# Kernel tuning notes

Measured on AMD Instinct MI355X. Metric: run time of the kernel, lower is better.

The kernel has to match this reference:

```python
import jax, jax.numpy as jnp
import numpy as np

# ---- model constants (match init_kwargs) ----
B, N, T, L = 16384, 32, 300, 1
DIM = 2                      # len(state_index)
DT = 1.0 / (T * L)           # dt = 1/(T*l)
STEPS = T * L                # Euler integration steps (time_steps = STEPS+1)
A_X = 1.0                    # canonical DMP phase constant
TAU = 1.0
HID = 64
OUT = N * DIM + DIM          # fc2_mean output size


def setup_inputs() -> dict:
    key = jax.random.key(0)
    ks = jax.random.split(key, 8)
    s = lambda i, shape, scale: jax.random.normal(ks[i], shape, jnp.float32) * scale
    inp = {
        "state": jax.random.normal(ks[0], (B, 3), jnp.float32),
        "fc1_w": s(1, (HID, 3), 0.3),
        "fc1_b": jnp.full((HID,), 0.1, jnp.float32),
        "fc2m_w": s(2, (OUT, HID), 0.1),
        "fc2m_b": jnp.full((OUT,), 0.1, jnp.float32),
        "sig_w": s(3, (DIM, HID), 0.1),
        "sig_b": jnp.zeros((DIM,), jnp.float32),
        "val_w": s(4, (DIM, HID), 0.1),
        "val_b": jnp.zeros((DIM,), jnp.float32),
    }
    # DMPParameters: gaussian RBF centers on exp-decayed phase, canonical widths
    c = jnp.exp(-A_X * jnp.linspace(0.0, 1.0, N))
    inp["dmp_c"] = c.astype(jnp.float32)
    inp["dmp_sigma2"] = (N ** 1.5 / c / A_X).astype(jnp.float32)
    return inp


def dmp_rollout(w, goal, y0, dy0, a_z, c, sigma2):
    """Euler rollout of DMP transformation system.
    w: [M,N] basis weights, goal/y0/dy0/a_z: [M] per-channel scalars.
    Returns Y, dY, ddY each [M, STEPS+1]."""
    z0 = dy0 * TAU
    b_z = a_z / 4.0

    def step(carry, _):
        x, y, z = carry
        x = x + (-A_X * x) * TAU * DT                       # phase update
        psi = jnp.exp(-0.5 * (x - c) ** 2 / sigma2)          # [N] gaussian RBF
        fx = (w @ psi) * x * (goal - y0) / jnp.sum(psi)      # [M] forcing term
        dz = a_z * (b_z * (goal - y) - z) + fx
        dy = z
        y = y + TAU * dy * DT
        z = z + TAU * dz * DT
        return (x, y, z), (y, dy * TAU, dz * TAU)

    _, (Ys, dYs, ddYs) = jax.lax.scan(
        step, (jnp.float32(1.0), y0, z0), None, length=STEPS)
    Y = jnp.concatenate([y0[None], Ys], axis=0).T            # [M, STEPS+1]
    dY = jnp.concatenate([dy0[None], dYs], axis=0).T
    ddY = jnp.concatenate([z0[None], ddYs], axis=0).T
    return Y, dY, ddY


def reference(state, fc1_w, fc1_b, fc2m_w, fc2m_b, sig_w, sig_b,
              val_w, val_b, dmp_c, dmp_sigma2):
    x = jnp.tanh(state @ fc1_w.T + fc1_b) * 0.1              # [B,64]
    y0 = state[:, :DIM].reshape(-1)                           # [M=B*DIM]
    dy0 = jnp.zeros_like(y0) + 0.01

    # value = fc2_value(x).repeat(1,T).view(-1,T,2).transpose(1,2) == broadcast over T
    v = x @ val_w.T + val_b                                   # [B,2]
    value = jnp.broadcast_to(v[:, :, None], (B, DIM, T))

    sigma = (jax.nn.sigmoid(x @ sig_w.T + sig_b) * 1.0 + 0.001).reshape(-1, DIM, 1)

    ndp_wg = x @ fc2m_w.T + fc2m_b                            # [B, 2N+2]
    goal = ndp_wg[:, :DIM].reshape(-1)                        # [M]
    w = ndp_wg[:, DIM:DIM * (N + 1)].reshape(-1, N)           # [M,N]
    a_z = jnp.clip(ndp_wg[:, -1], 0.5, 30.0)                  # learned a_z (az=True)
    a_z = jnp.broadcast_to(a_z[:, None], (B, DIM)).reshape(-1)

    Y, _, _ = dmp_rollout(w, goal, y0, dy0, a_z, dmp_c, dmp_sigma2)
    y = Y.reshape(B, DIM, -1)[:, :, ::L]                      # [B,2,T+1]
    a = y[:, :, 1:] - y[:, :, :-1]                            # [B,2,T]
    return (a, sigma, value)
```

## Files before the change

### kernel.cpp

```cpp
#include <hip/hip_runtime.h>
#include <hip/hip_bf16.h>

#define NB 32
#define TS 300
#define NBATCH 16384
#define DTF (1.0f/300.0f)
#define A_ELEMS (NBATCH*2*TS)

typedef __attribute__((ext_vector_type(8))) short bf16x8;
typedef __attribute__((ext_vector_type(4))) float f32x4;

static __device__ __forceinline__ ushort f2bf(float f) {
    union { __hip_bfloat16 h; ushort u; } cv;
    cv.h = __float2bfloat16(f);
    return cv.u;
}


__global__ __launch_bounds__(256) void k_head(
    const float* __restrict__ state,
    const float* __restrict__ fc1_w, const float* __restrict__ fc1_b,
    const float* __restrict__ fc2m_w, const float* __restrict__ fc2m_b,
    const float* __restrict__ sig_w, const float* __restrict__ sig_b,
    const float* __restrict__ val_w, const float* __restrict__ val_b,
    const float* __restrict__ dmp_c, const float* __restrict__ dmp_s2,
    float* __restrict__ sig_out, float* __restrict__ pbuf,
    ushort* __restrict__ wbuf16, uint4* __restrict__ wsPhi)
{
    const int tid = threadIdx.x;
    if (blockIdx.x == 256) {
        const float l2 = log2f(1.0f - DTF);
        for (int t = tid; t < 304; t += 256) {
            ushort row[NB];
            if (t < TS) {
                const float x = exp2f((float)(t + 1) * l2);
                float ps[NB]; float s = 0.0f;
                #pragma unroll
                for (int n = 0; n < NB; ++n) {
                    float d = x - dmp_c[n];
                    float p = __expf(-0.5f * d * d / dmp_s2[n]);
                    ps[n] = p; s += p;
                }
                const float inv = x / s;
                #pragma unroll
                for (int n = 0; n < NB; ++n) row[n] = f2bf(ps[n] * inv);
            } else {
                #pragma unroll
                for (int n = 0; n < NB; ++n) row[n] = 0;
            }
            #pragma unroll
            for (int g0 = 0; g0 < 4; ++g0) {
                union { ushort us[8]; uint4 v; } pk;
                #pragma unroll
                for (int e = 0; e < 8; ++e) pk.us[e] = row[g0*8 + e];
                wsPhi[(t >> 4)*64 + g0*16 + (t & 15)] = pk.v;
            }
        }
        return;
    }

    __shared__ uint4 bfr[640];
    __shared__ float f1s[64*4];
    __shared__ float biasl[80];
    __shared__ float hlds[4*16*68];
    __shared__ float ct[4*16*84];
    __shared__ float scl[4][16][2];

    const int wv  = tid >> 6;
    const int l   = tid & 63;
    const int b16 = l & 15;
    const int g   = l >> 4;

    for (int e = tid; e < 640; e += 256) {
        const int T = e >> 7, kk = (e >> 6) & 1, lane = e & 63;
        const int r = T*16 + (lane & 15);
        const int k0 = kk*32 + (lane >> 4)*8;
        union { ushort us[8]; uint4 v; } pk;
        if (r < 70) {
            const float* src = (r < 66) ? (fc2m_w + r*64 + k0)
                             : (r < 68) ? (sig_w + (r-66)*64 + k0)
                             : (val_w + (r-68)*64 + k0);
            #pragma unroll
            for (int i = 0; i < 8; ++i) pk.us[i] = f2bf(src[i]);
        } else {
            #pragma unroll
            for (int i = 0; i < 8; ++i) pk.us[i] = 0;
        }
        bfr[e] = pk.v;
    }
    if (tid < 64) {
        f1s[tid*4+0] = fc1_w[tid*3+0];
        f1s[tid*4+1] = fc1_w[tid*3+1];
        f1s[tid*4+2] = fc1_w[tid*3+2];
        f1s[tid*4+3] = fc1_b[tid];
    }
    if (tid < 80) biasl[tid] = (tid < 66) ? fc2m_b[tid] : (tid < 68) ? sig_b[tid-66]
                             : (tid < 70) ? val_b[tid-68] : 0.0f;
    __syncthreads();

    const int bbase = blockIdx.x*64 + wv*16;
    const int bglob = bbase + b16;
    const float s0 = state[bglob*3+0], s1 = state[bglob*3+1], s2 = state[bglob*3+2];

    float* hrow = hlds + wv*1088 + b16*68;
    #pragma unroll
    for (int i = 0; i < 16; ++i) {
        const int hid = g + 4*i;
        const float4 fw = *(const float4*)(f1s + hid*4);
        const float pre = fmaf(fw.x, s0, fmaf(fw.y, s1, fmaf(fw.z, s2, fw.w)));
        const float e = __expf(2.0f * pre);
        hrow[hid] = (1.0f - 2.0f/(e + 1.0f)) * 0.1f;
    }

    bf16x8 A0, A1;
    {
        const float* hr = hlds + wv*1088 + b16*68 + g*8;
        const float4 h0 = *(const float4*)(hr),      h1 = *(const float4*)(hr + 4);
        const float4 h2 = *(const float4*)(hr + 32), h3 = *(const float4*)(hr + 36);
        union { bf16x8 v; ushort u[8]; } p0, p1;
        p0.u[0]=f2bf(h0.x); p0.u[1]=f2bf(h0.y); p0.u[2]=f2bf(h0.z); p0.u[3]=f2bf(h0.w);
        p0.u[4]=f2bf(h1.x); p0.u[5]=f2bf(h1.y); p0.u[6]=f2bf(h1.z); p0.u[7]=f2bf(h1.w);
        p1.u[0]=f2bf(h2.x); p1.u[1]=f2bf(h2.y); p1.u[2]=f2bf(h2.z); p1.u[3]=f2bf(h2.w);
        p1.u[4]=f2bf(h3.x); p1.u[5]=f2bf(h3.y); p1.u[6]=f2bf(h3.z); p1.u[7]=f2bf(h3.w);
        A0 = p0.v; A1 = p1.v;
    }

    float* ctw = ct + wv*1344;
    const f32x4 zacc = {0.0f, 0.0f, 0.0f, 0.0f};
    #pragma unroll
    for (int T = 0; T < 5; ++T) {
        union { uint4 q; bf16x8 v; } B0, B1;
        B0.q = bfr[(T*2+0)*64 + l];
        B1.q = bfr[(T*2+1)*64 + l];
        f32x4 acc = __builtin_amdgcn_mfma_f32_16x16x32_bf16(A0, B0.v, zacc, 0, 0, 0);
        acc = __builtin_amdgcn_mfma_f32_16x16x32_bf16(A1, B1.v, acc, 0, 0, 0);
        const int r = T*16 + b16;
        const float bs = biasl[r];
        #pragma unroll
        for (int reg = 0; reg < 4; ++reg)
            ctw[(g*4 + reg)*84 + r] = acc[reg] + bs;
    }

    if (l < 32) {
        const int b = l & 15, d = l >> 4;
        const float goal = ctw[b*84 + d];
        const float y0 = state[(bbase + b)*3 + d];
        scl[wv][b][d] = DTF * (goal - y0);
    }

    uint* wout = (uint*)wbuf16;
    #pragma unroll 1
    for (int b = 0; b < 16; ++b) {
        if (l < 32) {
            const float2 wp = *(const float2*)(ctw + b*84 + 2 + 2*l);
            const float sc = scl[wv][b][l >> 4];
            wout[(bbase + b)*32 + l] =
                (uint)f2bf(wp.x * sc) | ((uint)f2bf(wp.y * sc) << 16);
        }
    }
    if (l < 16) {
        const float* cb = ctw + l*84;
        const float az = fminf(fmaxf(cb[65], 0.5f), 30.0f);
        const float y0 = state[(bbase + l)*3 + 0];
        *(float4*)(pbuf + ((bbase + l)*2 + 0)*4) = make_float4(cb[0], az, y0, cb[68]);
    } else if (l < 32) {
        const int b = l - 16;
        const float* cb = ctw + b*84;
        const float az = fminf(fmaxf(cb[65], 0.5f), 30.0f);
        const float y0 = state[(bbase + b)*3 + 1];
        *(float4*)(pbuf + ((bbase + b)*2 + 1)*4) = make_float4(cb[1], az, y0, cb[69]);
    } else if (l < 48) {
        const int b = l - 32;
        const float* cb = ctw + b*84;
        const float sg0 = 1.0f / (1.0f + __expf(-cb[66])) + 0.001f;
        const float sg1 = 1.0f / (1.0f + __expf(-cb[67])) + 0.001f;
        *(float2*)(sig_out + (bbase + b)*2) = make_float2(sg0, sg1);
    }
}

__global__ __launch_bounds__(256) void k_roll(
    const uint4* __restrict__ wsPhi, const float* __restrict__ pbuf,
    const ushort* __restrict__ wbuf16, float* __restrict__ a_out,
    float* __restrict__ v_out)
{
    const int tid = threadIdx.x;
    const int wv = tid >> 6;
    const int j  = tid & 63;
    const int ch = j & 15;
    const int g  = j >> 4;
    const int m  = (blockIdx.x << 6) + (wv << 4) + ch;

    const float4 pp = *(const float4*)(pbuf + m*4);
    const float az = pp.y;
    const float Ac = (DTF * 0.25f) * az * az;
    const float OmB = fmaf(-DTF, az, 1.0f);
    const float c0 = Ac * pp.x;
    float y = pp.z;
    float z = 0.01f;
    const f32x4 cvec = {c0, c0, c0, c0};

    const bf16x8 wb = *(const bf16x8*)(wbuf16 + m*NB + g*8);
    const bf16x8* ap = (const bf16x8*)wsPhi;
    bf16x8 af = ap[j];

    float* aptr = a_out + m*TS + (g << 2);
    float* vptr = v_out + m*TS + (g << 2);
    const float4 vsp = make_float4(pp.w, pp.w, pp.w, pp.w);

    for (int c = 0; c < 19; ++c) {
        const bool st = (c < 18) | (g < 3);
        if (st) { *(float4*)vptr = vsp; }
        vptr += 16;

        f32x4 facc = __builtin_amdgcn_mfma_f32_16x16x32_bf16(af, wb, cvec, 0, 0, 0);
        if (c < 18) af = ap[(c + 1)*64 + j];

        float F[16];
        #pragma unroll
        for (int q = 0; q < 4; ++q) {
            float a = facc[q], b = facc[q];
            asm volatile("v_permlane16_swap_b32 %0, %1" : "+v"(a), "+v"(b));
            float a2 = a, b2 = b;
            asm volatile("v_permlane32_swap_b32 %0, %1" : "+v"(a), "+v"(a2));
            asm volatile("v_permlane32_swap_b32 %0, %1" : "+v"(b), "+v"(b2));
            F[0*4+q] = a; F[1*4+q] = b; F[2*4+q] = a2; F[3*4+q] = b2;
        }

        float avq[4];
        #pragma unroll
        for (int i = 0; i < 16; ++i) {
            const float t2 = fmaf(-Ac, y, F[i]);
            if (g == (i >> 2)) avq[i & 3] = z;
            y = fmaf(DTF, z, y);
            z = fmaf(OmB, z, t2);
        }

        if (st) {
            *(float4*)aptr = make_float4(avq[0]*DTF, avq[1]*DTF, avq[2]*DTF, avq[3]*DTF);
        }
        aptr += 16;
    }
}

extern "C" void kernel_launch(void* const* d_in, const int* in_sizes, int n_in,
                              void* d_out, int out_size, void* d_ws, size_t ws_size,
                              hipStream_t stream) {
    (void)in_sizes; (void)n_in; (void)out_size; (void)ws_size;
    const float* state  = (const float*)d_in[0];
    const float* fc1_w  = (const float*)d_in[1];
    const float* fc1_b  = (const float*)d_in[2];
    const float* fc2m_w = (const float*)d_in[3];
    const float* fc2m_b = (const float*)d_in[4];
    const float* sig_w  = (const float*)d_in[5];
    const float* sig_b  = (const float*)d_in[6];
    const float* val_w  = (const float*)d_in[7];
    const float* val_b  = (const float*)d_in[8];
    const float* dmp_c  = (const float*)d_in[9];
    const float* dmp_s2 = (const float*)d_in[10];

    float* out     = (float*)d_out;
    float* a_out   = out;
    float* sig_out = out + A_ELEMS;
    float* v_out   = out + A_ELEMS + NBATCH*2;

    char* ws = (char*)d_ws;
    uint4*  wsPhi  = (uint4*)ws;
    float*  pbuf   = (float*)(ws + 32768);
    ushort* wbuf16 = (ushort*)(ws + 557056);

    k_head<<<dim3(257), dim3(256), 0, stream>>>(state, fc1_w, fc1_b, fc2m_w, fc2m_b,
                                                sig_w, sig_b, val_w, val_b,
                                                dmp_c, dmp_s2,
                                                sig_out, pbuf, wbuf16, wsPhi);
    k_roll<<<dim3(512), dim3(256), 0, stream>>>(wsPhi, pbuf, wbuf16, a_out, v_out);
}
```

Before: 30.03 us.

## Fuse head and rollout kernels into one cooperative launch with grid sync

```diff
diff --git a/kernel.cpp b/kernel.cpp
--- a/kernel.cpp
+++ b/kernel.cpp
@@ -1,5 +1,8 @@
 #include <hip/hip_runtime.h>
 #include <hip/hip_bf16.h>
+#include <hip/hip_cooperative_groups.h>
+
+namespace cg = cooperative_groups;
 
 #define NB 32
 #define TS 300
@@ -17,7 +20,7 @@
 }
 
 
-__global__ __launch_bounds__(256) void k_head(
+__global__ __launch_bounds__(256) void k_all(
     const float* __restrict__ state,
     const float* __restrict__ fc1_w, const float* __restrict__ fc1_b,
     const float* __restrict__ fc2m_w, const float* __restrict__ fc2m_b,
@@ -25,10 +28,20 @@
     const float* __restrict__ val_w, const float* __restrict__ val_b,
     const float* __restrict__ dmp_c, const float* __restrict__ dmp_s2,
     float* __restrict__ sig_out, float* __restrict__ pbuf,
-    ushort* __restrict__ wbuf16, uint4* __restrict__ wsPhi)
+    ushort* __restrict__ wbuf16, uint4* __restrict__ wsPhi,
+    float* __restrict__ a_out, float* __restrict__ v_out)
 {
+    __shared__ uint4 bfr[640];
+    __shared__ float f1s[64*4];
+    __shared__ float biasl[80];
+    __shared__ float hlds[4*16*68];
+    __shared__ float ct[4*16*84];
+    __shared__ float scl[4][16][2];
+
     const int tid = threadIdx.x;
-    if (blockIdx.x == 256) {
+    const int bid = blockIdx.x;
+
+    if (bid == 256) {
         const float l2 = log2f(1.0f - DTF);
         for (int t = tid; t < 304; t += 256) {
             ushort row[NB];
@@ -56,189 +69,178 @@
                 wsPhi[(t >> 4)*64 + g0*16 + (t & 15)] = pk.v;
             }
         }
-        return;
-    }
-
-    __shared__ uint4 bfr[640];
-    __shared__ float f1s[64*4];
-    __shared__ float biasl[80];
-    __shared__ float hlds[4*16*68];
-    __shared__ float ct[4*16*84];
-    __shared__ float scl[4][16][2];
-
-    const int wv  = tid >> 6;
-    const int l   = tid & 63;
-    const int b16 = l & 15;
-    const int g   = l >> 4;
-
-    for (int e = tid; e < 640; e += 256) {
-        const int T = e >> 7, kk = (e >> 6) & 1, lane = e & 63;
-        const int r = T*16 + (lane & 15);
-        const int k0 = kk*32 + (lane >> 4)*8;
-        union { ushort us[8]; uint4 v; } pk;
-        if (r < 70) {
-            const float* src = (r < 66) ? (fc2m_w + r*64 + k0)
-                             : (r < 68) ? (sig_w + (r-66)*64 + k0)
-                             : (val_w + (r-68)*64 + k0);
-            #pragma unroll
-            for (int i = 0; i < 8; ++i) pk.us[i] = f2bf(src[i]);
-        } else {
-            #pragma unroll
-            for (int i = 0; i < 8; ++i) pk.us[i] = 0;
-        }
-        bfr[e] = pk.v;
-    }
-    if (tid < 64) {
-        f1s[tid*4+0] = fc1_w[tid*3+0];
-        f1s[tid*4+1] = fc1_w[tid*3+1];
-        f1s[tid*4+2] = fc1_w[tid*3+2];
-        f1s[tid*4+3] = fc1_b[tid];
-    }
-    if (tid < 80) biasl[tid] = (tid < 66) ? fc2m_b[tid] : (tid < 68) ? sig_b[tid-66]
-                             : (tid < 70) ? val_b[tid-68] : 0.0f;
-    __syncthreads();
-
-    const int bbase = blockIdx.x*64 + wv*16;
-    const int bglob = bbase + b16;
-    const float s0 = state[bglob*3+0], s1 = state[bglob*3+1], s2 = state[bglob*3+2];
-
-    float* hrow = hlds + wv*1088 + b16*68;
-    #pragma unroll
-    for (int i = 0; i < 16; ++i) {
-        const int hid = g + 4*i;
-        const float4 fw = *(const float4*)(f1s + hid*4);
-        const float pre = fmaf(fw.x, s0, fmaf(fw.y, s1, fmaf(fw.z, s2, fw.w)));
-        const float e = __expf(2.0f * pre);
-        hrow[hid] = (1.0f - 2.0f/(e + 1.0f)) * 0.1f;
-    }
-
-    bf16x8 A0, A1;
-    {
-        const float* hr = hlds + wv*1088 + b16*68 + g*8;
-        const float4 h0 = *(const float4*)(hr),      h1 = *(const float4*)(hr + 4);
-        const float4 h2 = *(const float4*)(hr + 32), h3 = *(const float4*)(hr + 36);
-        union { bf16x8 v; ushort u[8]; } p0, p1;
-        p0.u[0]=f2bf(h0.x); p0.u[1]=f2bf(h0.y); p0.u[2]=f2bf(h0.z); p0.u[3]=f2bf(h0.w);
-        p0.u[4]=f2bf(h1.x); p0.u[5]=f2bf(h1.y); p0.u[6]=f2bf(h1.z); p0.u[7]=f2bf(h1.w);
-        p1.u[0]=f2bf(h2.x); p1.u[1]=f2bf(h2.y); p1.u[2]=f2bf(h2.z); p1.u[3]=f2bf(h2.w);
-        p1.u[4]=f2bf(h3.x); p1.u[5]=f2bf(h3.y); p1.u[6]=f2bf(h3.z); p1.u[7]=f2bf(h3.w);
-        A0 = p0.v; A1 = p1.v;
-    }
-
-    float* ctw = ct + wv*1344;
-    const f32x4 zacc = {0.0f, 0.0f, 0.0f, 0.0f};
-    #pragma unroll
-    for (int T = 0; T < 5; ++T) {
-        union { uint4 q; bf16x8 v; } B0, B1;
-        B0.q = bfr[(T*2+0)*64 + l];
-        B1.q = bfr[(T*2+1)*64 + l];
-        f32x4 acc = __builtin_amdgcn_mfma_f32_16x16x32_bf16(A0, B0.v, zacc, 0, 0, 0);
-        acc = __builtin_amdgcn_mfma_f32_16x16x32_bf16(A1, B1.v, acc, 0, 0, 0);
-        const int r = T*16 + b16;
-        const float bs = biasl[r];
-        #pragma unroll
-        for (int reg = 0; reg < 4; ++reg)
-            ctw[(g*4 + reg)*84 + r] = acc[reg] + bs;
-    }
-
-    if (l < 32) {
-        const int b = l & 15, d = l >> 4;
-        const float goal = ctw[b*84 + d];
-        const float y0 = state[(bbase + b)*3 + d];
-        scl[wv][b][d] = DTF * (goal - y0);
-    }
-
-    uint* wout = (uint*)wbuf16;
-    #pragma unroll 1
-    for (int b = 0; b < 16; ++b) {
-        if (l < 32) {
-            const float2 wp = *(const float2*)(ctw + b*84 + 2 + 2*l);
-            const float sc = scl[wv][b][l >> 4];
-            wout[(bbase + b)*32 + l] =
-                (uint)f2bf(wp.x * sc) | ((uint)f2bf(wp.y * sc) << 16);
-        }
-    }
-    if (l < 16) {
-        const float* cb = ctw + l*84;
-        const float az = fminf(fmaxf(cb[65], 0.5f), 30.0f);
-        const float y0 = state[(bbase + l)*3 + 0];
-        *(float4*)(pbuf + ((bbase + l)*2 + 0)*4) = make_float4(cb[0], az, y0, cb[68]);
-    } else if (l < 32) {
-        const int b = l - 16;
-        const float* cb = ctw + b*84;
-        const float az = fminf(fmaxf(cb[65], 0.5f), 30.0f);
-        const float y0 = state[(bbase + b)*3 + 1];
-        *(float4*)(pbuf + ((bbase + b)*2 + 1)*4) = make_float4(cb[1], az, y0, cb[69]);
-    } else if (l < 48) {
-        const int b = l - 32;
-        const float* cb = ctw + b*84;
-        const float sg0 = 1.0f / (1.0f + __expf(-cb[66])) + 0.001f;
-        const float sg1 = 1.0f / (1.0f + __expf(-cb[67])) + 0.001f;
-        *(float2*)(sig_out + (bbase + b)*2) = make_float2(sg0, sg1);
-    }
-}
-
-__global__ __launch_bounds__(256) void k_roll(
-    const uint4* __restrict__ wsPhi, const float* __restrict__ pbuf,
-    const ushort* __restrict__ wbuf16, float* __restrict__ a_out,
-    float* __restrict__ v_out)
-{
-    const int tid = threadIdx.x;
-    const int wv = tid >> 6;
-    const int j  = tid & 63;
-    const int ch = j & 15;
-    const int g  = j >> 4;
-    const int m  = (blockIdx.x << 6) + (wv << 4) + ch;
-
-    const float4 pp = *(const float4*)(pbuf + m*4);
-    const float az = pp.y;
-    const float Ac = (DTF * 0.25f) * az * az;
-    const float OmB = fmaf(-DTF, az, 1.0f);
-    const float c0 = Ac * pp.x;
-    float y = pp.z;
-    float z = 0.01f;
-    const f32x4 cvec = {c0, c0, c0, c0};
-
-    const bf16x8 wb = *(const bf16x8*)(wbuf16 + m*NB + g*8);
-    const bf16x8* ap = (const bf16x8*)wsPhi;
-    bf16x8 af = ap[j];
-
-    float* aptr = a_out + m*TS + (g << 2);
-    float* vptr = v_out + m*TS + (g << 2);
-    const float4 vsp = make_float4(pp.w, pp.w, pp.w, pp.w);
-
-    for (int c = 0; c < 19; ++c) {
-        const bool st = (c < 18) | (g < 3);
-        if (st) { *(float4*)vptr = vsp; }
-        vptr += 16;
-
-        f32x4 facc = __builtin_amdgcn_mfma_f32_16x16x32_bf16(af, wb, cvec, 0, 0, 0);
-        if (c < 18) af = ap[(c + 1)*64 + j];
-
-        float F[16];
-        #pragma unroll
-        for (int q = 0; q < 4; ++q) {
-            float a = facc[q], b = facc[q];
-            asm volatile("v_permlane16_swap_b32 %0, %1" : "+v"(a), "+v"(b));
-            float a2 = a, b2 = b;
-            asm volatile("v_permlane32_swap_b32 %0, %1" : "+v"(a), "+v"(a2));
-            asm volatile("v_permlane32_swap_b32 %0, %1" : "+v"(b), "+v"(b2));
-            F[0*4+q] = a; F[1*4+q] = b; F[2*4+q] = a2; F[3*4+q] = b2;
-        }
-
-        float avq[4];
+    } else if (bid < 256) {
+        const int wv  = tid >> 6;
+        const int l   = tid & 63;
+        const int b16 = l & 15;
+        const int g   = l >> 4;
+
+        for (int e = tid; e < 640; e += 256) {
+            const int T = e >> 7, kk = (e >> 6) & 1, lane = e & 63;
+            const int r = T*16 + (lane & 15);
+            const int k0 = kk*32 + (lane >> 4)*8;
+            union { ushort us[8]; uint4 v; } pk;
+            if (r < 70) {
+                const float* src = (r < 66) ? (fc2m_w + r*64 + k0)
+                                 : (r < 68) ? (sig_w + (r-66)*64 + k0)
+                                 : (val_w + (r-68)*64 + k0);
+                #pragma unroll
+                for (int i = 0; i < 8; ++i) pk.us[i] = f2bf(src[i]);
+            } else {
+                #pragma unroll
+                for (int i = 0; i < 8; ++i) pk.us[i] = 0;
+            }
+            bfr[e] = pk.v;
+        }
+        if (tid < 64) {
+            f1s[tid*4+0] = fc1_w[tid*3+0];
+            f1s[tid*4+1] = fc1_w[tid*3+1];
+            f1s[tid*4+2] = fc1_w[tid*3+2];
+            f1s[tid*4+3] = fc1_b[tid];
+        }
+        if (tid < 80) biasl[tid] = (tid < 66) ? fc2m_b[tid] : (tid < 68) ? sig_b[tid-66]
+                                 : (tid < 70) ? val_b[tid-68] : 0.0f;
+        __syncthreads();
+
+        const int bbase = bid*64 + wv*16;
+        const int bglob = bbase + b16;
+        const float s0 = state[bglob*3+0], s1 = state[bglob*3+1], s2 = state[bglob*3+2];
+
+        float* hrow = hlds + wv*1088 + b16*68;
         #pragma unroll
         for (int i = 0; i < 16; ++i) {
-            const float t2 = fmaf(-Ac, y, F[i]);
-            if (g == (i >> 2)) avq[i & 3] = z;
-            y = fmaf(DTF, z, y);
-            z = fmaf(OmB, z, t2);
-        }
-
-        if (st) {
-            *(float4*)aptr = make_float4(avq[0]*DTF, avq[1]*DTF, avq[2]*DTF, avq[3]*DTF);
-        }
-        aptr += 16;
+            const int hid = g + 4*i;
+            const float4 fw = *(const float4*)(f1s + hid*4);
+            const float pre = fmaf(fw.x, s0, fmaf(fw.y, s1, fmaf(fw.z, s2, fw.w)));
+            const float e = __expf(2.0f * pre);
+            hrow[hid] = (1.0f - 2.0f/(e + 1.0f)) * 0.1f;
+        }
+
+        bf16x8 A0, A1;
+        {
+            const float* hr = hlds + wv*1088 + b16*68 + g*8;
+            const float4 h0 = *(const float4*)(hr),      h1 = *(const float4*)(hr + 4);
+            const float4 h2 = *(const float4*)(hr + 32), h3 = *(const float4*)(hr + 36);
+            union { bf16x8 v; ushort u[8]; } p0, p1;
+            p0.u[0]=f2bf(h0.x); p0.u[1]=f2bf(h0.y); p0.u[2]=f2bf(h0.z); p0.u[3]=f2bf(h0.w);
+            p0.u[4]=f2bf(h1.x); p0.u[5]=f2bf(h1.y); p0.u[6]=f2bf(h1.z); p0.u[7]=f2bf(h1.w);
+            p1.u[0]=f2bf(h2.x); p1.u[1]=f2bf(h2.y); p1.u[2]=f2bf(h2.z); p1.u[3]=f2bf(h2.w);
+            p1.u[4]=f2bf(h3.x); p1.u[5]=f2bf(h3.y); p1.u[6]=f2bf(h3.z); p1.u[7]=f2bf(h3.w);
+            A0 = p0.v; A1 = p1.v;
+        }
+
+        float* ctw = ct + wv*1344;
+        const f32x4 zacc = {0.0f, 0.0f, 0.0f, 0.0f};
+        #pragma unroll
+        for (int T = 0; T < 5; ++T) {
+            union { uint4 q; bf16x8 v; } B0, B1;
+            B0.q = bfr[(T*2+0)*64 + l];
+            B1.q = bfr[(T*2+1)*64 + l];
+            f32x4 acc = __builtin_amdgcn_mfma_f32_16x16x32_bf16(A0, B0.v, zacc, 0, 0, 0);
+            acc = __builtin_amdgcn_mfma_f32_16x16x32_bf16(A1, B1.v, acc, 0, 0, 0);
+            const int r = T*16 + b16;
+            const float bs = biasl[r];
+            #pragma unroll
+            for (int reg = 0; reg < 4; ++reg)
+                ctw[(g*4 + reg)*84 + r] = acc[reg] + bs;
+        }
+
+        if (l < 32) {
+            const int b = l & 15, d = l >> 4;
+            const float goal = ctw[b*84 + d];
+            const float y0 = state[(bbase + b)*3 + d];
+            scl[wv][b][d] = DTF * (goal - y0);
+        }
+
+        uint* wout = (uint*)wbuf16;
+        #pragma unroll 1
+        for (int b = 0; b < 16; ++b) {
+            if (l < 32) {
+                const float2 wp = *(const float2*)(ctw + b*84 + 2 + 2*l);
+                const float sc = scl[wv][b][l >> 4];
+                wout[(bbase + b)*32 + l] =
+                    (uint)f2bf(wp.x * sc) | ((uint)f2bf(wp.y * sc) << 16);
+            }
+        }
+        if (l < 16) {
+            const float* cb = ctw + l*84;
+            const float az = fminf(fmaxf(cb[65], 0.5f), 30.0f);
+            const float y0 = state[(bbase + l)*3 + 0];
+            *(float4*)(pbuf + ((bbase + l)*2 + 0)*4) = make_float4(cb[0], az, y0, cb[68]);
+        } else if (l < 32) {
+            const int b = l - 16;
+            const float* cb = ctw + b*84;
+            const float az = fminf(fmaxf(cb[65], 0.5f), 30.0f);
+            const float y0 = state[(bbase + b)*3 + 1];
+            *(float4*)(pbuf + ((bbase + b)*2 + 1)*4) = make_float4(cb[1], az, y0, cb[69]);
+        } else if (l < 48) {
+            const int b = l - 32;
+            const float* cb = ctw + b*84;
+            const float sg0 = 1.0f / (1.0f + __expf(-cb[66])) + 0.001f;
+            const float sg1 = 1.0f / (1.0f + __expf(-cb[67])) + 0.001f;
+            *(float2*)(sig_out + (bbase + b)*2) = make_float2(sg0, sg1);
+        }
+    }
+
+    cg::this_grid().sync();
+
+    {
+        const int wv = tid >> 6;
+        const int j  = tid & 63;
+        const int ch = j & 15;
+        const int g  = j >> 4;
+        const int m  = (bid << 6) + (wv << 4) + ch;
+
+        const float4 pp = *(const float4*)(pbuf + m*4);
+        const float az = pp.y;
+        const float Ac = (DTF * 0.25f) * az * az;
+        const float OmB = fmaf(-DTF, az, 1.0f);
+        const float c0 = Ac * pp.x;
+        float y = pp.z;
+        float z = 0.01f;
+        const f32x4 cvec = {c0, c0, c0, c0};
+
+        const bf16x8 wb = *(const bf16x8*)(wbuf16 + m*NB + g*8);
+        const bf16x8* ap = (const bf16x8*)wsPhi;
+        bf16x8 af = ap[j];
+
+        float* aptr = a_out + m*TS + (g << 2);
+        float* vptr = v_out + m*TS + (g << 2);
+        const float4 vsp = make_float4(pp.w, pp.w, pp.w, pp.w);
+
+        for (int c = 0; c < 19; ++c) {
+            const bool st = (c < 18) | (g < 3);
+            if (st) { *(float4*)vptr = vsp; }
+            vptr += 16;
+
+            f32x4 facc = __builtin_amdgcn_mfma_f32_16x16x32_bf16(af, wb, cvec, 0, 0, 0);
+            if (c < 18) af = ap[(c + 1)*64 + j];
+
+            float F[16];
+            #pragma unroll
+            for (int q = 0; q < 4; ++q) {
+                float a = facc[q], b = facc[q];
+                asm volatile("v_permlane16_swap_b32 %0, %1" : "+v"(a), "+v"(b));
+                float a2 = a, b2 = b;
+                asm volatile("v_permlane32_swap_b32 %0, %1" : "+v"(a), "+v"(a2));
+                asm volatile("v_permlane32_swap_b32 %0, %1" : "+v"(b), "+v"(b2));
+                F[0*4+q] = a; F[1*4+q] = b; F[2*4+q] = a2; F[3*4+q] = b2;
+            }
+
+            float avq[4];
+            #pragma unroll
+            for (int i = 0; i < 16; ++i) {
+                const float t2 = fmaf(-Ac, y, F[i]);
+                if (g == (i >> 2)) avq[i & 3] = z;
+                y = fmaf(DTF, z, y);
+                z = fmaf(OmB, z, t2);
+            }
+
+            if (st) {
+                *(float4*)aptr = make_float4(avq[0]*DTF, avq[1]*DTF, avq[2]*DTF, avq[3]*DTF);
+            }
+            aptr += 16;
+        }
     }
 }
 
@@ -268,9 +270,12 @@
     float*  pbuf   = (float*)(ws + 32768);
     ushort* wbuf16 = (ushort*)(ws + 557056);
 
-    k_head<<<dim3(257), dim3(256), 0, stream>>>(state, fc1_w, fc1_b, fc2m_w, fc2m_b,
-                                                sig_w, sig_b, val_w, val_b,
-                                                dmp_c, dmp_s2,
-                                                sig_out, pbuf, wbuf16, wsPhi);
-    k_roll<<<dim3(512), dim3(256), 0, stream>>>(wsPhi, pbuf, wbuf16, a_out, v_out);
+    void* args[] = {
+        (void*)&state, (void*)&fc1_w, (void*)&fc1_b, (void*)&fc2m_w, (void*)&fc2m_b,
+        (void*)&sig_w, (void*)&sig_b, (void*)&val_w, (void*)&val_b,
+        (void*)&dmp_c, (void*)&dmp_s2,
+        (void*)&sig_out, (void*)&pbuf, (void*)&wbuf16, (void*)&wsPhi,
+        (void*)&a_out, (void*)&v_out
+    };
+    hipLaunchCooperativeKernel((void*)k_all, dim3(512), dim3(256), args, 0, stream);
 }
```

After: 78.65 us. +161.9%, slower.
